# Optimization experiments

Hardware: AMD Instinct MI355X
Metric: run time of the kernel (lower is better)

Reference implementation:

```python
import jax, jax.numpy as jnp
import numpy as np

IGNORE = 255
MAX_CLIP_DIST = 20.0
MAX_N_RATIO = 0.01
LB_SMOOTH = 0.2
N_DIR = 8
MAX_DIS = 1e5
X_RANGE = [1, -1, 0, 0, -1, 1, -1, 1, 0]
Y_RANGE = [0, 0, -1, 1, 1, 1, -1, -1, 0]


def _kl(a, b):
    # sum_c softmax(b) * (log_softmax(b) - log_softmax(a)) over channel axis
    return jnp.sum(jax.nn.softmax(b, -1) * (jax.nn.log_softmax(b, -1) - jax.nn.log_softmax(a, -1)), axis=-1)


def gt2boundary(gt):
    ud = jnp.pad(gt[:, 1:, :] - gt[:, :-1, :], ((0, 0), (0, 1), (0, 0))) != 0
    lr = jnp.pad(gt[:, :, 1:] - gt[:, :, :-1], ((0, 0), (0, 0), (0, 1))) != 0
    return ud | lr | (gt == IGNORE)


def edt(bound):
    # Exact Euclidean distance to nearest True pixel (Meijster two-phase). bound: [B,H,W] bool.
    B, H, W = bound.shape
    INF = jnp.float32(1e6)
    col = jnp.where(bound, 0.0, INF).transpose(1, 0, 2)  # [H,B,W]

    def step(c, r):
        d = jnp.minimum(r, c + 1.0)
        return d, d

    _, dn = jax.lax.scan(step, jnp.full((B, W), INF), col)
    _, up = jax.lax.scan(step, jnp.full((B, W), INF), col[::-1])
    G = jnp.minimum(dn, up[::-1]).transpose(1, 0, 2)  # [B,H,W] vertical distance
    G2 = G * G
    j = jnp.arange(W, dtype=jnp.float32)
    off = (j[:, None] - j[None, :]) ** 2  # [W,W]
    rows = G2.reshape(-1, W)
    CH = 128
    pad = (-rows.shape[0]) % CH
    rows = jnp.pad(rows, ((0, pad), (0, 0)))
    chunks = rows.reshape(-1, CH, W)

    def f(c):  # [CH,W] -> [CH,W]
        return jnp.min(c[:, None, :] + off[None, :, :], axis=-1)

    D2 = jax.lax.map(f, chunks).reshape(-1, W)[: B * H].reshape(B, H, W)
    return jnp.sqrt(D2)


def get_dist_maps(gt_bound):
    d = jnp.maximum(edt(gt_bound) - 1.0, 0.0)  # distance-1 outside boundary, 0 on it
    any_b = jnp.any(gt_bound, axis=(1, 2))
    return jnp.where(any_b[:, None, None], d, 0.0)


def logits2boundary(logits):
    B, H, W, C = logits.shape
    max_N = float(H * W) * MAX_N_RATIO
    kl_ud = _kl(logits[:, 1:], logits[:, :-1])      # [B,H-1,W]
    kl_lr = _kl(logits[:, :, 1:], logits[:, :, :-1])  # [B,H,W-1]
    kl = jnp.pad(kl_ud, ((0, 0), (0, 1), (0, 0))) + jnp.pad(kl_lr, ((0, 0), (0, 0), (0, 1)))
    kl = jax.lax.stop_gradient(kl)  # boundary mask carries no gradient
    eps = jax.lax.while_loop(
        lambda e: jnp.sum(kl > e) > max_N,
        lambda e: e * jnp.float32(1.2),
        jnp.float32(1e-5),
    )
    bin_ = (kl > eps).astype(jnp.float32)[..., None]
    ker = jnp.ones((3, 3, 1, 1), jnp.float32)
    dil = jax.lax.conv_general_dilated(bin_, ker, (1, 1), 'SAME',
                                       dimension_numbers=('NHWC', 'HWIO', 'NHWC'))
    return dil[..., 0] > 0


def direction_loss(dist_map, pred_bound, logits):
    B, H, W, C = logits.shape
    dist_p = jnp.pad(dist_map, ((0, 0), (1, 1), (1, 1)), constant_values=MAX_DIS)
    log_p = jnp.pad(logits, ((0, 0), (1, 1), (1, 1), (0, 0)))
    dists, kls = [], []
    for dx, dy in zip(X_RANGE, Y_RANGE):
        dists.append(dist_p[:, 1 + dx:1 + dx + H, 1 + dy:1 + dy + W])
        if dx != 0 or dy != 0:
            nb = jax.lax.stop_gradient(log_p[:, 1 + dx:1 + dx + H, 1 + dy:1 + dy + W, :])
            kls.append(_kl(logits, nb))  # kl_div(center, neighbor)
    dists = jnp.stack(dists, -1)   # [B,H,W,9]
    kl_maps = jnp.stack(kls, -1)   # [B,H,W,8]
    dir_gt = jnp.argmin(dists, -1)
    valid = pred_bound & (dir_gt != 8)
    w = jnp.clip(dist_map, 0.0, MAX_CLIP_DIST) / MAX_CLIP_DIST
    logp = jax.nn.log_softmax(kl_maps, -1)
    lbl = jax.nn.one_hot(dir_gt, N_DIR, dtype=logp.dtype) * (1.0 - LB_SMOOTH) + LB_SMOOTH / N_DIR
    ce = -jnp.sum(lbl * logp, -1)
    vf = valid.astype(jnp.float32)
    return jnp.sum(ce * w * vf) / jnp.maximum(jnp.sum(vf), 1.0)


def setup_inputs() -> dict:
    key = jax.random.key(0)
    k1, k2 = jax.random.split(key)
    logits = jax.random.normal(k1, (4, 512, 512, 19), dtype=jnp.float32)
    coarse = jax.random.randint(k2, (4, 32, 32), 0, 19)
    target = jnp.repeat(jnp.repeat(coarse, 16, axis=1), 16, axis=2).astype(jnp.int32)
    return {"logits": logits, "target": target}


def reference(logits, target):
    gt_bound = gt2boundary(target)
    dist_maps = get_dist_maps(gt_bound)
    pred_bound = logits2boundary(logits)
    return direction_loss(dist_maps, pred_bound, logits)
```

## Files before the change

### kernel.cpp

```cpp
#include <hip/hip_runtime.h>
#include <math.h>

#define NB 4
#define NH 512
#define NW 512
#define NC 19
#define NPIX (NB*NH*NW)
#define TS 16
#define NLAD 128
#define INF6 1.0e6f
#define MAXDIS 1.0e5f
#define NWRD 16
#define NREP 8
#define HSTRIDE 132
#define NBND 128
#define NVD (NB*NH)
#define NKL (NPIX/512)
#define NT3 ((NW/TS)*(NH/TS)*NB)
#define NZERO2 (NREP*HSTRIDE)

struct Lad { float v[NLAD]; };
static constexpr Lad make_lad() {
    Lad t{};
    float e = 1e-5f;
    for (int k = 0; k < NLAD; ++k) { t.v[k] = e; e *= 1.2f; }
    return t;
}
__constant__ Lad LADC = make_lad();

__device__ __forceinline__ void load19(const float* __restrict__ base, float (&v)[NC]) {
    float4 q0 = *reinterpret_cast<const float4*>(base);
    float4 q1 = *reinterpret_cast<const float4*>(base + 4);
    float4 q2 = *reinterpret_cast<const float4*>(base + 8);
    float4 q3 = *reinterpret_cast<const float4*>(base + 12);
    float4 q4 = *reinterpret_cast<const float4*>(base + 15);
    v[0]=q0.x; v[1]=q0.y; v[2]=q0.z; v[3]=q0.w;
    v[4]=q1.x; v[5]=q1.y; v[6]=q1.z; v[7]=q1.w;
    v[8]=q2.x; v[9]=q2.y; v[10]=q2.z; v[11]=q2.w;
    v[12]=q3.x; v[13]=q3.y; v[14]=q3.z; v[15]=q3.w;
    v[16]=q4.y; v[17]=q4.z; v[18]=q4.w;
}

__global__ __launch_bounds__(256) void k1_kernel(const int* __restrict__ tgt,
                                                 const float* __restrict__ logits,
                                                 unsigned int* __restrict__ maskw,
                                                 float* __restrict__ lsem,
                                                 unsigned int* __restrict__ zbuf) {
    const int tid = threadIdx.x;
    if (blockIdx.x < NBND) {
        if (blockIdx.x == 0) {
            for (int k = tid; k < NZERO2; k += 256) zbuf[k] = 0u;
        }
        const int cidx = blockIdx.x * 256 + tid;
        const int j = cidx & (NW - 1);
        const int w = (cidx >> 9) & (NWRD - 1);
        const int b = cidx >> 13;
        const int* t = tgt + (size_t)b * NH * NW;
        unsigned int mask = 0u;
        const int i0 = w * 32;
        int cur = t[(size_t)i0 * NW + j];
        for (int k = 0; k < 32; ++k) {
            int i = i0 + k;
            int nxt = (i + 1 < NH) ? t[(size_t)(i + 1) * NW + j] : cur;
            bool bnd = (cur == 255);
            if (i + 1 < NH && nxt != cur) bnd = true;
            if (j + 1 < NW && t[(size_t)i * NW + j + 1] != cur) bnd = true;
            if (bnd) mask |= (1u << k);
            cur = nxt;
        }
        maskw[cidx] = mask;
    } else {
        const int p = (blockIdx.x - NBND) * 256 + tid;
        float v[NC];
        load19(logits + (size_t)p * NC, v);
        float mx = v[0];
#pragma unroll
        for (int c = 1; c < NC; ++c) mx = fmaxf(mx, v[c]);
        float se = 0.f;
#pragma unroll
        for (int c = 0; c < NC; ++c) se += expf(v[c] - mx);
        lsem[p] = mx + logf(se);
    }
}

__global__ __launch_bounds__(512) void k2_kernel(const unsigned int* __restrict__ maskw,
                                                 const float* __restrict__ logits,
                                                 const float* __restrict__ lsem,
                                                 float* __restrict__ dist,
                                                 float* __restrict__ klb,
                                                 unsigned int* __restrict__ hist) {
    __shared__ unsigned int smw[NWRD][NW];
    __shared__ float srow[NW];
    __shared__ unsigned int anyw[8];
    __shared__ float lad[NLAD];
    __shared__ unsigned int lh[NLAD + 1];
    const int tid = threadIdx.x;

    if (blockIdx.x < NVD) {
        const int row = blockIdx.x;
        const int b = row >> 9;
        const int i = row & (NH - 1);
        const unsigned int* mcol = maskw + (size_t)b * NWRD * NW;
        unsigned int acc = 0u;
#pragma unroll
        for (int w = 0; w < NWRD; ++w) {
            unsigned int v = mcol[w * NW + tid];
            smw[w][tid] = v;
            acc |= v;
        }
        unsigned long long bal = __ballot(acc != 0u);
        if ((tid & 63) == 0) anyw[tid >> 6] = (bal != 0ull) ? 1u : 0u;

        const int wi = i >> 5, bi = i & 31;
        int down = 1 << 20;
        unsigned int m = smw[wi][tid] & ((2u << bi) - 1u);
        if (m) down = bi - (31 - __clz(m));
        else {
            for (int w = wi - 1; w >= 0; --w) {
                unsigned int mm = smw[w][tid];
                if (mm) { down = bi + 32 * (wi - w) - (31 - __clz(mm)); break; }
            }
        }
        int up = 1 << 20;
        unsigned int mu = smw[wi][tid] & ~((1u << bi) - 1u);
        if (mu) up = (__ffs(mu) - 1) - bi;
        else {
            for (int w = wi + 1; w < NWRD; ++w) {
                unsigned int mm = smw[w][tid];
                if (mm) { up = 32 * (w - wi) + (__ffs(mm) - 1) - bi; break; }
            }
        }
        int gi = min(down, up);
        float G = (gi >= (1 << 20)) ? INF6 : (float)gi;
        srow[tid] = G * G;
        __syncthreads();
        bool has = (anyw[0] | anyw[1] | anyw[2] | anyw[3] |
                    anyw[4] | anyw[5] | anyw[6] | anyw[7]) != 0u;
        float best = srow[tid];
        for (int r = 1; r < NW; ++r) {
            float rr = (float)(r * r);
            if (rr >= best) break;
            int jl = tid - r, jr = tid + r;
            if (jl >= 0) best = fminf(best, srow[jl] + rr);
            if (jr < NW) best = fminf(best, srow[jr] + rr);
        }
        dist[(size_t)row * NW + tid] = has ? fmaxf(sqrtf(best) - 1.f, 0.f) : 0.f;
    } else {
        if (tid < NLAD) lad[tid] = LADC.v[tid];
        if (tid < NLAD + 1) lh[tid] = 0u;
        __syncthreads();

        const int kb = blockIdx.x - NVD;
        const int row = ((kb & 7) << 8) | (kb >> 3);
        const int p = row * 512 + tid;
        const int j = tid;
        const int i = row & (NH - 1);
        const bool hasr = (j < NW - 1), hasd = (i < NH - 1);
        const float lse_c = lsem[p];
        const float lse_r = hasr ? lsem[p + 1] : 0.f;
        const float lse_d = hasd ? lsem[p + NW] : 0.f;
        const float* base = logits + (size_t)p * NC;
        const int offr = hasr ? NC : 0;
        const int offd = hasd ? NW * NC : 0;

        float lc[NC];
        load19(base, lc);
        float pc[NC];
        float negH = 0.f;
#pragma unroll
        for (int c = 0; c < NC; ++c) {
            float s = lc[c] - lse_c;
            float e = expf(s);
            pc[c] = e;
            negH += e * s;
        }
        float lr[NC];
        load19(base + offr, lr);
        float dotr = 0.f;
#pragma unroll
        for (int c = 0; c < NC; ++c) dotr += pc[c] * lr[c];
        float ld[NC];
        load19(base + offd, ld);
        float dotd = 0.f;
#pragma unroll
        for (int c = 0; c < NC; ++c) dotd += pc[c] * ld[c];

        float kl = 0.f;
        if (hasd) kl += negH + lse_d - dotd;
        if (hasr) kl += negH + lse_r - dotr;
        klb[p] = kl;

        int lo = 0, hi = NLAD;
        while (lo < hi) { int mid = (lo + hi) >> 1; if (kl > lad[mid]) lo = mid + 1; else hi = mid; }
        atomicAdd(&lh[lo], 1u);
        __syncthreads();
        if (tid < NLAD + 1 && lh[tid])
            atomicAdd(&hist[(blockIdx.x & (NREP - 1)) * HSTRIDE + tid], lh[tid]);
    }
}

__global__ __launch_bounds__(256) void k3_kernel(const float* __restrict__ klb,
                                                 const float* __restrict__ dist,
                                                 const float* __restrict__ logits,
                                                 const float* __restrict__ lsem,
                                                 const unsigned int* __restrict__ hist,
                                                 float* __restrict__ partials,
                                                 unsigned int* __restrict__ bcnt) {
    __shared__ unsigned int suf[NLAD + 1];
    __shared__ unsigned int wcnt[4];
    __shared__ float epsS;
    __shared__ float klT[18][19];
    __shared__ float dsT[18][19];
    __shared__ unsigned int ent[256];
    __shared__ unsigned int nvS;
    __shared__ float rs[256];
    const int tid = threadIdx.x;
    if (tid < NLAD + 1) {
        unsigned int s = 0;
        for (int r = 0; r < NREP; ++r) s += hist[r * HSTRIDE + tid];
        suf[tid] = s;
    }
    if (tid == 0) nvS = 0u;
    if (tid < 4) wcnt[tid] = 0u;

    const int b = blockIdx.z;
    const int i0 = blockIdx.y * TS;
    const int j0 = blockIdx.x * TS;
    const float* klp = klb + (size_t)b * NH * NW;
    const float* dp = dist + (size_t)b * NH * NW;

    for (int t = tid; t < 324; t += 256) {
        const int r = t / 18, c = t % 18;
        const int ii = i0 - 1 + r, jj = j0 - 1 + c;
        const bool inb = (ii >= 0 && ii < NH && jj >= 0 && jj < NW);
        klT[r][c] = inb ? klp[(size_t)ii * NW + jj] : -1.f;
        dsT[r][c] = inb ? dp[(size_t)ii * NW + jj] : MAXDIS;
    }
    __syncthreads();

#pragma unroll
    for (int step = 1; step <= 128; step <<= 1) {
        unsigned int val = 0u;
        if (tid <= NLAD) {
            val = suf[tid];
            if (tid + step <= NLAD) val += suf[tid + step];
        }
        __syncthreads();
        if (tid <= NLAD) suf[tid] = val;
        __syncthreads();
    }
    {
        bool flag = (tid < NLAD - 1) && ((float)suf[tid + 1] > 2621.44f);
        unsigned long long mk = __ballot(flag);
        if ((tid & 63) == 0) wcnt[tid >> 6] = (unsigned int)__popcll(mk);
        __syncthreads();
        if (tid == 0) epsS = LADC.v[wcnt[0] + wcnt[1] + wcnt[2] + wcnt[3]];
        __syncthreads();
    }
    const float eps = epsS;

    const int ty = tid >> 4, tx = tid & 15;
    const int i = i0 + ty, j = j0 + tx;

    bool pb = false;
#pragma unroll
    for (int r = 0; r < 3; ++r)
#pragma unroll
        for (int c = 0; c < 3; ++c)
            if (klT[ty + r][tx + c] > eps) pb = true;

    const int dxs[9] = {1, -1, 0, 0, -1, 1, -1, 1, 0};
    const int dys[9] = {0, 0, -1, 1, 1, 1, -1, -1, 0};
    float best = MAXDIS; int gidx = 0;
#pragma unroll
    for (int k = 0; k < 9; ++k) {
        float v = dsT[ty + 1 + dxs[k]][tx + 1 + dys[k]];
        if (k == 0) { best = v; gidx = 0; }
        else if (v < best) { best = v; gidx = k; }
    }
    const bool valid = pb && (gidx != 8);
    const int pix = (b * NH + i) * NW + j;

    const int lane = tid & 63;
    unsigned long long mk = __ballot(valid);
    int cnt = __popcll(mk);
    unsigned int base = 0u;
    if (lane == 0 && cnt) base = atomicAdd(&nvS, (unsigned int)cnt);
    base = (unsigned int)__shfl((int)base, 0, 64);
    if (valid)
        ent[base + (unsigned int)__popcll(mk & ((1ull << lane) - 1ull))] =
            (unsigned int)pix | ((unsigned int)gidx << 20) | ((unsigned int)tid << 24);
    __syncthreads();
    const int nv = (int)nvS;

    float acc = 0.f;
    const int grp = tid >> 3, d = tid & 7;
    for (int e = grp; e < nv; e += 32) {
        const unsigned int w = ent[e];
        const int epix = (int)(w & (NPIX - 1));
        const int egidx = (int)((w >> 20) & 15u);
        const int etid = (int)(w >> 24);
        const int ej = epix & (NW - 1);
        const int ei = (epix >> 9) & (NH - 1);

        const unsigned int DXP = (2u<<0)|(0u<<2)|(1u<<4)|(1u<<6)|(0u<<8)|(2u<<10)|(0u<<12)|(2u<<14);
        const unsigned int DYP = (1u<<0)|(1u<<2)|(0u<<4)|(2u<<6)|(2u<<8)|(2u<<10)|(0u<<12)|(0u<<14);
        const int dx = (int)((DXP >> (2 * d)) & 3u) - 1;
        const int dy = (int)((DYP >> (2 * d)) & 3u) - 1;
        const int ii = ei + dx, jj = ej + dy;
        const bool inb = (ii >= 0 && ii < NH && jj >= 0 && jj < NW);

        const float lse_c = lsem[epix];
        const float* lcp = logits + (size_t)epix * NC;
        float lc[NC];
        load19(lcp, lc);
        float sumlc = 0.f;
#pragma unroll
        for (int c = 0; c < NC; ++c) sumlc += lc[c];

        float klm;
        if (inb) {
            const int npix = epix + dx * NW + dy;
            const float lse_n = lsem[npix];
            const float* lnp = logits + (size_t)npix * NC;
            float ln[NC];
            load19(lnp, ln);
            float negH = 0.f, dot = 0.f;
#pragma unroll
            for (int c = 0; c < NC; ++c) {
                float sv = ln[c] - lse_n;
                float p = expf(sv);
                negH += p * sv;
                dot += p * lc[c];
            }
            klm = negH + lse_c - dot;
        } else {
            klm = -logf(19.f) + lse_c - sumlc / 19.f;
        }

        float m2 = klm;
#pragma unroll
        for (int o = 4; o > 0; o >>= 1) m2 = fmaxf(m2, __shfl_xor(m2, o, 8));
        float ex = expf(klm - m2);
        float s2 = ex;
#pragma unroll
        for (int o = 4; o > 0; o >>= 1) s2 += __shfl_xor(s2, o, 8);
        float lse = m2 + logf(s2);
        float lp = klm - lse;
        float slp = lp;
#pragma unroll
        for (int o = 4; o > 0; o >>= 1) slp += __shfl_xor(slp, o, 8);
        float kg = (d == egidx) ? lp : 0.f;
#pragma unroll
        for (int o = 4; o > 0; o >>= 1) kg += __shfl_xor(kg, o, 8);

        if (d == 0) {
            float ce = -(0.2f / 8.f) * slp - 0.8f * kg;
            float wgt = fminf(dsT[(etid >> 4) + 1][(etid & 15) + 1], 20.f) / 20.f;
            acc += ce * wgt;
        }
    }
    rs[tid] = acc;
    __syncthreads();
    for (int q = 128; q > 0; q >>= 1) {
        if (tid < q) rs[tid] += rs[tid + q];
        __syncthreads();
    }
    if (tid == 0) {
        const int bid = (blockIdx.z * gridDim.y + blockIdx.y) * gridDim.x + blockIdx.x;
        partials[bid] = rs[0];
        bcnt[bid] = (unsigned int)nv;
    }
}

__global__ __launch_bounds__(256) void k4_kernel(const float* __restrict__ partials,
                                                 const unsigned int* __restrict__ bcnt,
                                                 float* __restrict__ out) {
    __shared__ float r1[256];
    __shared__ unsigned int r2[256];
    const int tid = threadIdx.x;
    float s = 0.f;
    unsigned int c = 0u;
#pragma unroll
    for (int q = 0; q < NT3 / 256; ++q) {
        s += partials[tid + q * 256];
        c += bcnt[tid + q * 256];
    }
    r1[tid] = s; r2[tid] = c;
    __syncthreads();
    for (int q = 128; q > 0; q >>= 1) {
        if (tid < q) { r1[tid] += r1[tid + q]; r2[tid] += r2[tid + q]; }
        __syncthreads();
    }
    if (tid == 0) out[0] = r1[0] / fmaxf((float)r2[0], 1.f);
}

extern "C" void kernel_launch(void* const* d_in, const int* in_sizes, int n_in,
                              void* d_out, int out_size, void* d_ws, size_t ws_size,
                              hipStream_t stream) {
    const float* logits = (const float*)d_in[0];
    const int* target = (const int*)d_in[1];
    float* out = (float*)d_out;

    float* fws = (float*)d_ws;
    float* distb = fws;
    float* klb = fws + NPIX;
    float* lsem = fws + 2 * (size_t)NPIX;
    unsigned int* hist = (unsigned int*)(fws + 3 * (size_t)NPIX);
    float* partials = (float*)(hist + NREP * HSTRIDE);
    unsigned int* bcnt = (unsigned int*)(partials + NT3);
    unsigned int* maskw = bcnt + NT3;

    k1_kernel<<<NBND + NPIX / 256, 256, 0, stream>>>(target, logits, maskw, lsem, hist);
    k2_kernel<<<NVD + NKL, 512, 0, stream>>>(maskw, logits, lsem, distb, klb, hist);
    dim3 tiles(NW / TS, NH / TS, NB);
    k3_kernel<<<tiles, 256, 0, stream>>>(klb, distb, logits, lsem, hist,
                                         partials, bcnt);
    k4_kernel<<<1, 256, 0, stream>>>(partials, bcnt, out);
}
```

Before: 82.30 us.

## Fuse log-sum-exp into KL kernel, two rows per block, drop lsem buffer

Removes the separate per-pixel log-sum-exp pass from k1 and the lsem workspace. The KL stage now handles two rows per block and computes LSE in registers, sharing the right neighbour's LSE through shared memory. The second row's vertical neighbour is reused from the already loaded row. k3 recomputes LSE for the centre and neighbour pixels from the loaded logits. This cuts one full read of the 80MB logits tensor plus the lsem write and reads, at the cost of extra exp work and higher register pressure in k2.

```diff
diff --git a/kernel.cpp b/kernel.cpp
--- a/kernel.cpp
+++ b/kernel.cpp
@@ -13,9 +13,8 @@
 #define NWRD 16
 #define NREP 8
 #define HSTRIDE 132
-#define NBND 128
 #define NVD (NB*NH)
-#define NKL (NPIX/512)
+#define NKL2 (NB*NH/2)
 #define NT3 ((NW/TS)*(NH/TS)*NB)
 #define NZERO2 (NREP*HSTRIDE)
 
@@ -41,57 +40,53 @@
     v[16]=q4.y; v[17]=q4.z; v[18]=q4.w;
 }
 
-__global__ __launch_bounds__(256) void k1_kernel(const int* __restrict__ tgt,
-                                                 const float* __restrict__ logits,
-                                                 unsigned int* __restrict__ maskw,
-                                                 float* __restrict__ lsem,
-                                                 unsigned int* __restrict__ zbuf) {
+__device__ __forceinline__ float lse19(const float (&v)[NC]) {
+    float mx = v[0];
+#pragma unroll
+    for (int c = 1; c < NC; ++c) mx = fmaxf(mx, v[c]);
+    float se = 0.f;
+#pragma unroll
+    for (int c = 0; c < NC; ++c) se += expf(v[c] - mx);
+    return mx + logf(se);
+}
+
+__global__ __launch_bounds__(64) void k1_kernel(const int* __restrict__ tgt,
+                                                unsigned int* __restrict__ maskw,
+                                                unsigned int* __restrict__ zbuf) {
     const int tid = threadIdx.x;
-    if (blockIdx.x < NBND) {
-        if (blockIdx.x == 0) {
-            for (int k = tid; k < NZERO2; k += 256) zbuf[k] = 0u;
-        }
-        const int cidx = blockIdx.x * 256 + tid;
-        const int j = cidx & (NW - 1);
-        const int w = (cidx >> 9) & (NWRD - 1);
-        const int b = cidx >> 13;
-        const int* t = tgt + (size_t)b * NH * NW;
-        unsigned int mask = 0u;
-        const int i0 = w * 32;
-        int cur = t[(size_t)i0 * NW + j];
-        for (int k = 0; k < 32; ++k) {
-            int i = i0 + k;
-            int nxt = (i + 1 < NH) ? t[(size_t)(i + 1) * NW + j] : cur;
-            bool bnd = (cur == 255);
-            if (i + 1 < NH && nxt != cur) bnd = true;
-            if (j + 1 < NW && t[(size_t)i * NW + j + 1] != cur) bnd = true;
-            if (bnd) mask |= (1u << k);
-            cur = nxt;
-        }
-        maskw[cidx] = mask;
-    } else {
-        const int p = (blockIdx.x - NBND) * 256 + tid;
-        float v[NC];
-        load19(logits + (size_t)p * NC, v);
-        float mx = v[0];
-#pragma unroll
-        for (int c = 1; c < NC; ++c) mx = fmaxf(mx, v[c]);
-        float se = 0.f;
-#pragma unroll
-        for (int c = 0; c < NC; ++c) se += expf(v[c] - mx);
-        lsem[p] = mx + logf(se);
-    }
+    if (blockIdx.x == 0) {
+        for (int k = tid; k < NZERO2; k += 64) zbuf[k] = 0u;
+    }
+    const int cidx = blockIdx.x * 64 + tid;
+    const int j = cidx & (NW - 1);
+    const int w = (cidx >> 9) & (NWRD - 1);
+    const int b = cidx >> 13;
+    const int* t = tgt + (size_t)b * NH * NW;
+    unsigned int mask = 0u;
+    const int i0 = w * 32;
+    int cur = t[(size_t)i0 * NW + j];
+    for (int k = 0; k < 32; ++k) {
+        int i = i0 + k;
+        int nxt = (i + 1 < NH) ? t[(size_t)(i + 1) * NW + j] : cur;
+        bool bnd = (cur == 255);
+        if (i + 1 < NH && nxt != cur) bnd = true;
+        if (j + 1 < NW && t[(size_t)i * NW + j + 1] != cur) bnd = true;
+        if (bnd) mask |= (1u << k);
+        cur = nxt;
+    }
+    maskw[cidx] = mask;
 }
 
 __global__ __launch_bounds__(512) void k2_kernel(const unsigned int* __restrict__ maskw,
                                                  const float* __restrict__ logits,
-                                                 const float* __restrict__ lsem,
                                                  float* __restrict__ dist,
                                                  float* __restrict__ klb,
                                                  unsigned int* __restrict__ hist) {
     __shared__ unsigned int smw[NWRD][NW];
     __shared__ float srow[NW];
     __shared__ unsigned int anyw[8];
+    __shared__ float lseA[NW];
+    __shared__ float lseB[NW];
     __shared__ float lad[NLAD];
     __shared__ unsigned int lh[NLAD + 1];
     const int tid = threadIdx.x;
@@ -148,51 +143,87 @@
     } else {
         if (tid < NLAD) lad[tid] = LADC.v[tid];
         if (tid < NLAD + 1) lh[tid] = 0u;
-        __syncthreads();
 
         const int kb = blockIdx.x - NVD;
-        const int row = ((kb & 7) << 8) | (kb >> 3);
-        const int p = row * 512 + tid;
+        const int rp = ((kb & 7) << 7) | (kb >> 3);
+        const int r0 = rp * 2;
+        const int i0 = r0 & (NH - 1);
         const int j = tid;
-        const int i = row & (NH - 1);
-        const bool hasr = (j < NW - 1), hasd = (i < NH - 1);
-        const float lse_c = lsem[p];
-        const float lse_r = hasr ? lsem[p + 1] : 0.f;
-        const float lse_d = hasd ? lsem[p + NW] : 0.f;
-        const float* base = logits + (size_t)p * NC;
+        const size_t p0 = (size_t)r0 * NW + j;
+        const size_t p1 = p0 + NW;
+        const bool hasr = (j < NW - 1);
+        const bool hasd1 = (i0 + 1 < NH - 1);
+        const float* b0 = logits + p0 * NC;
+        const float* b1 = logits + p1 * NC;
         const int offr = hasr ? NC : 0;
-        const int offd = hasd ? NW * NC : 0;
-
-        float lc[NC];
-        load19(base, lc);
-        float pc[NC];
-        float negH = 0.f;
-#pragma unroll
-        for (int c = 0; c < NC; ++c) {
-            float s = lc[c] - lse_c;
-            float e = expf(s);
-            pc[c] = e;
-            negH += e * s;
-        }
-        float lr[NC];
-        load19(base + offr, lr);
-        float dotr = 0.f;
-#pragma unroll
-        for (int c = 0; c < NC; ++c) dotr += pc[c] * lr[c];
-        float ld[NC];
-        load19(base + offd, ld);
-        float dotd = 0.f;
-#pragma unroll
-        for (int c = 0; c < NC; ++c) dotd += pc[c] * ld[c];
-
-        float kl = 0.f;
-        if (hasd) kl += negH + lse_d - dotd;
-        if (hasr) kl += negH + lse_r - dotr;
-        klb[p] = kl;
-
-        int lo = 0, hi = NLAD;
-        while (lo < hi) { int mid = (lo + hi) >> 1; if (kl > lad[mid]) lo = mid + 1; else hi = mid; }
-        atomicAdd(&lh[lo], 1u);
+        const int offd1 = hasd1 ? NW * NC : 0;
+
+        float lc0[NC];
+        load19(b0, lc0);
+        float lc1[NC];
+        load19(b1, lc1);
+        const float lse0 = lse19(lc0);
+        const float lse1 = lse19(lc1);
+        lseA[tid] = lse0;
+        lseB[tid] = lse1;
+        __syncthreads();
+        const float lse_r0 = hasr ? lseA[tid + 1] : 0.f;
+        const float lse_r1 = hasr ? lseB[tid + 1] : 0.f;
+
+        {
+            float pc[NC];
+            float negH = 0.f;
+#pragma unroll
+            for (int c = 0; c < NC; ++c) {
+                float s = lc0[c] - lse0;
+                float e = expf(s);
+                pc[c] = e;
+                negH += e * s;
+            }
+            float lr[NC];
+            load19(b0 + offr, lr);
+            float dotr = 0.f;
+#pragma unroll
+            for (int c = 0; c < NC; ++c) dotr += pc[c] * lr[c];
+            float dotd = 0.f;
+#pragma unroll
+            for (int c = 0; c < NC; ++c) dotd += pc[c] * lc1[c];
+            float kl = negH + lse1 - dotd;
+            if (hasr) kl += negH + lse_r0 - dotr;
+            klb[p0] = kl;
+            int lo = 0, hi = NLAD;
+            while (lo < hi) { int mid = (lo + hi) >> 1; if (kl > lad[mid]) lo = mid + 1; else hi = mid; }
+            atomicAdd(&lh[lo], 1u);
+        }
+        {
+            float ld1[NC];
+            load19(b1 + offd1, ld1);
+            const float lse2 = hasd1 ? lse19(ld1) : 0.f;
+            float pc[NC];
+            float negH = 0.f;
+#pragma unroll
+            for (int c = 0; c < NC; ++c) {
+                float s = lc1[c] - lse1;
+                float e = expf(s);
+                pc[c] = e;
+                negH += e * s;
+            }
+            float lr[NC];
+            load19(b1 + offr, lr);
+            float dotr = 0.f;
+#pragma unroll
+            for (int c = 0; c < NC; ++c) dotr += pc[c] * lr[c];
+            float dotd = 0.f;
+#pragma unroll
+            for (int c = 0; c < NC; ++c) dotd += pc[c] * ld1[c];
+            float kl = 0.f;
+            if (hasd1) kl += negH + lse2 - dotd;
+            if (hasr) kl += negH + lse_r1 - dotr;
+            klb[p1] = kl;
+            int lo = 0, hi = NLAD;
+            while (lo < hi) { int mid = (lo + hi) >> 1; if (kl > lad[mid]) lo = mid + 1; else hi = mid; }
+            atomicAdd(&lh[lo], 1u);
+        }
         __syncthreads();
         if (tid < NLAD + 1 && lh[tid])
             atomicAdd(&hist[(blockIdx.x & (NREP - 1)) * HSTRIDE + tid], lh[tid]);
@@ -202,7 +233,6 @@
 __global__ __launch_bounds__(256) void k3_kernel(const float* __restrict__ klb,
                                                  const float* __restrict__ dist,
                                                  const float* __restrict__ logits,
-                                                 const float* __restrict__ lsem,
                                                  const unsigned int* __restrict__ hist,
                                                  float* __restrict__ partials,
                                                  unsigned int* __restrict__ bcnt) {
@@ -310,21 +340,21 @@
         const int ii = ei + dx, jj = ej + dy;
         const bool inb = (ii >= 0 && ii < NH && jj >= 0 && jj < NW);
 
-        const float lse_c = lsem[epix];
         const float* lcp = logits + (size_t)epix * NC;
         float lc[NC];
         load19(lcp, lc);
         float sumlc = 0.f;
 #pragma unroll
         for (int c = 0; c < NC; ++c) sumlc += lc[c];
+        const float lse_c = lse19(lc);
 
         float klm;
         if (inb) {
             const int npix = epix + dx * NW + dy;
-            const float lse_n = lsem[npix];
             const float* lnp = logits + (size_t)npix * NC;
             float ln[NC];
             load19(lnp, ln);
+            const float lse_n = lse19(ln);
             float negH = 0.f, dot = 0.f;
 #pragma unroll
             for (int c = 0; c < NC; ++c) {
@@ -405,16 +435,14 @@
     float* fws = (float*)d_ws;
     float* distb = fws;
     float* klb = fws + NPIX;
-    float* lsem = fws + 2 * (size_t)NPIX;
-    unsigned int* hist = (unsigned int*)(fws + 3 * (size_t)NPIX);
+    unsigned int* hist = (unsigned int*)(fws + 2 * (size_t)NPIX);
     float* partials = (float*)(hist + NREP * HSTRIDE);
     unsigned int* bcnt = (unsigned int*)(partials + NT3);
     unsigned int* maskw = bcnt + NT3;
 
-    k1_kernel<<<NBND + NPIX / 256, 256, 0, stream>>>(target, logits, maskw, lsem, hist);
-    k2_kernel<<<NVD + NKL, 512, 0, stream>>>(maskw, logits, lsem, distb, klb, hist);
+    k1_kernel<<<NB * NWRD * NW / 64, 64, 0, stream>>>(target, maskw, hist);
+    k2_kernel<<<NVD + NKL2, 512, 0, stream>>>(maskw, logits, distb, klb, hist);
     dim3 tiles(NW / TS, NH / TS, NB);
-    k3_kernel<<<tiles, 256, 0, stream>>>(klb, distb, logits, lsem, hist,
-                                         partials, bcnt);
+    k3_kernel<<<tiles, 256, 0, stream>>>(klb, distb, logits, hist, partials, bcnt);
     k4_kernel<<<1, 256, 0, stream>>>(partials, bcnt, out);
 }
```

Result: slower. 91.03 us (+10.6%).
